# Kernel optimization log

Measured on AMD Instinct MI355X. Metric: run time of the kernel, lower is better.

The kernel has to match this reference:

```python
import jax, jax.numpy as jnp
import numpy as np

B, L, C, H = 32, 641, 768, 12
MEM = 128  # memory slots K; state token at index K; tokens are causal after that


def _block_mask(L, K):
    # rows i attend to cols j per FusedAttention:
    #  memory rows (i<K): attend to memory+state (j<=K)
    #  state row (i==K): attends to everything
    #  token rows (i>K): attend to memory+state (j<=K) and causally to tokens (K<j<=i)
    i = jnp.arange(L)[:, None]
    j = jnp.arange(L)[None, :]
    mem_rows = (i < K) & (j <= K)
    state_row = (i == K)
    tok_rows = (i > K) & ((j <= K) | ((j > K) & (j <= i)))
    return mem_rows | state_row | tok_rows  # (L, L) bool


def setup_inputs() -> dict:
    key = jax.random.key(0)
    k1, k2, k3 = jax.random.split(key, 3)
    x = jax.random.normal(k1, (B, L, C), dtype=jnp.float32)
    W_attn = jax.random.normal(k2, (C, 3 * C), dtype=jnp.float32) * 0.02
    W_proj = jax.random.normal(k3, (C, C), dtype=jnp.float32) * 0.02
    return {"x": x, "W_attn": W_attn, "W_proj": W_proj, "mem_size": MEM}


def reference(x, W_attn, W_proj, mem_size):
    Bb, Ll, Cc = x.shape
    hd = Cc // H
    qkv = x @ W_attn  # (B, L, 3C)
    q, k, v = jnp.split(qkv, 3, axis=-1)
    # (B, H, L, hd)
    q = q.reshape(Bb, Ll, H, hd).transpose(0, 2, 1, 3)
    k = k.reshape(Bb, Ll, H, hd).transpose(0, 2, 1, 3)
    v = v.reshape(Bb, Ll, H, hd).transpose(0, 2, 1, 3)
    mask = _block_mask(Ll, mem_size)  # (L, L)
    scale = 1.0 / jnp.sqrt(jnp.asarray(hd, dtype=x.dtype))
    att = jnp.einsum("bhqd,bhkd->bhqk", q, k) * scale
    att = jnp.where(mask[None, None, :, :], att, jnp.asarray(-jnp.inf, att.dtype))
    att = jax.nn.softmax(att, axis=-1)
    y = jnp.einsum("bhqk,bhkd->bhqd", att, v)
    y = y.transpose(0, 2, 1, 3).reshape(Bb, Ll, Cc)
    return y @ W_proj
```

## Files before the change

kernel.cpp:

```cpp
#include <hip/hip_runtime.h>
#include <stdint.h>

#define B_SZ 32
#define L_SZ 641
#define C_SZ 768
#define H_SZ 12
#define HD 64
#define MEMK 128
#define M_REAL (B_SZ * L_SZ)
#define M_PAD 20608
#define MT256 81
#define N_QKV (3 * C_SZ)
#define NQP 6
#define QK_STRIDE 1536
#define VT_STRIDE 648
#define SCL_LOG2E 0.18033688f
#define FIXED_MAX 8.0f

typedef __attribute__((ext_vector_type(8))) short short8;
typedef __attribute__((ext_vector_type(4))) float f32x4;
typedef __attribute__((ext_vector_type(4))) unsigned short ushort4v;

__device__ inline unsigned short f2bf(float x) {
  union { float f; uint32_t u; } v; v.f = x;
  uint32_t r = v.u + 0x7fffu + ((v.u >> 16) & 1u);
  return (unsigned short)(r >> 16);
}
__device__ inline float bf2f(short v) {
  union { float f; uint32_t u; } x; x.u = ((uint32_t)(unsigned short)v) << 16;
  return x.f;
}

__device__ inline void gload_lds16(const void* g, void* l) {
  __builtin_amdgcn_global_load_lds(
      (const __attribute__((address_space(1))) uint32_t*)g,
      (__attribute__((address_space(3))) uint32_t*)l, 16, 0, 0);
}

__global__ __launch_bounds__(256) void k_conv_x(const float* __restrict__ src,
                                                unsigned short* __restrict__ dst,
                                                int n4) {
  int i = blockIdx.x * 256 + threadIdx.x;
  if (i >= n4) return;
  float4 v = *(const float4*)(src + (size_t)i * 4);
  ushort4v o = { f2bf(v.x), f2bf(v.y), f2bf(v.z), f2bf(v.w) };
  int m = (unsigned)i / 192u;
  int k = (i - m * 192) * 4;
  int kk = k ^ ((m & 7) << 3);
  *(ushort4v*)(dst + (size_t)m * C_SZ + kk) = o;
}

__global__ __launch_bounds__(256) void k_transpose_bf16(const float* __restrict__ src,
                                                        unsigned short* __restrict__ dst,
                                                        int R, int Ccol,
                                                        float scale, int scale_cmax) {
  __shared__ float tile[32][33];
  int c0 = blockIdx.x * 32, r0 = blockIdx.y * 32;
  int tx = threadIdx.x & 31, ty = threadIdx.x >> 5;
  for (int i = ty; i < 32; i += 8)
    tile[i][tx] = src[(size_t)(r0 + i) * Ccol + c0 + tx];
  __syncthreads();
  float sc = (c0 < scale_cmax) ? scale : 1.0f;
  for (int i = ty; i < 32; i += 8) {
    int c = c0 + i;
    int r = (r0 + tx) ^ ((c & 7) << 3);
    dst[(size_t)c * R + r] = f2bf(tile[tx][i] * sc);
  }
}

template <int MODE>
__global__ __launch_bounds__(512, 2) void k_gemm(const short* __restrict__ A,
                                                 const short* __restrict__ Bt,
                                                 void* __restrict__ Cp,
                                                 short* __restrict__ vt,
                                                 int Mreal, int N, int K) {
  __shared__ short As[2][256 * 64];
  __shared__ short Bs[2][256 * 64];
  int nwg = gridDim.x;
  int qq = nwg >> 3, rr = nwg & 7;
  int x8 = blockIdx.x & 7, i8 = blockIdx.x >> 3;
  int wg = (x8 < rr ? x8 * (qq + 1) : rr * (qq + 1) + (x8 - rr) * qq) + i8;
  const int tiles_n = N >> 8;
  int tm = wg / tiles_n, tn = wg % tiles_n;
  int m0 = tm << 8, n0 = tn << 8;
  int tid = threadIdx.x;
  int lane = tid & 63, wave = tid >> 6;
  int wr = wave >> 2, wc = wave & 3;
  int l15 = lane & 15, g = lane >> 4;
  int gswz = (l15 & 7) << 4;

  f32x4 acc[8][4];
  f32x4 z = {0.f, 0.f, 0.f, 0.f};
#pragma unroll
  for (int i2 = 0; i2 < 8; ++i2)
#pragma unroll
    for (int j2 = 0; j2 < 4; ++j2) acc[i2][j2] = z;

  int srow = wave * 8 + (lane >> 3);
  int scol = (lane & 7) * 8;

#define STAGE(K0, BUF)                                                        \
  {                                                                           \
    _Pragma("unroll")                                                         \
    for (int s = 0; s < 4; ++s) {                                             \
      int ar = m0 + s * 64 + srow;                                            \
      if (ar >= M_PAD) ar = M_PAD - 1;      \
      gload_lds16(A + (size_t)ar * K + ((K0) + scol),                         \
                  (char*)As[BUF] + s * 8192 + wave * 1024);                   \
      gload_lds16(Bt + (size_t)(n0 + s * 64 + srow) * K + ((K0) + scol),      \
                  (char*)Bs[BUF] + s * 8192 + wave * 1024);                   \
    }                                                                         \
  }

  STAGE(0, 0);
  STAGE(64, 1);
  int nk = K >> 6;
  for (int t = 0; t < nk; ++t) {
    int buf = t & 1;
    if (t + 1 < nk) {
      asm volatile("s_waitcnt vmcnt(8)" ::: "memory");
    } else {
      asm volatile("s_waitcnt vmcnt(0)" ::: "memory");
    }
    __builtin_amdgcn_s_barrier();
#pragma unroll
    for (int ks = 0; ks < 2; ++ks) {
      short8 a[8], b[4];
      if (MODE == 3) {
#pragma unroll
        for (int j = 0; j < 8; ++j)
          a[j] = *(const short8*)((char*)Bs[buf] +
                      (wr * 128 + j * 16 + l15) * 128 + ((ks * 64 + g * 16) ^ gswz));
#pragma unroll
        for (int i = 0; i < 4; ++i)
          b[i] = *(const short8*)((char*)As[buf] +
                      (wc * 64 + i * 16 + l15) * 128 + ((ks * 64 + g * 16) ^ gswz));
      } else {
#pragma unroll
        for (int mf = 0; mf < 8; ++mf)
          a[mf] = *(const short8*)((char*)As[buf] +
                      (wr * 128 + mf * 16 + l15) * 128 + ((ks * 64 + g * 16) ^ gswz));
#pragma unroll
        for (int nf = 0; nf < 4; ++nf)
          b[nf] = *(const short8*)((char*)Bs[buf] +
                      (wc * 64 + nf * 16 + l15) * 128 + ((ks * 64 + g * 16) ^ gswz));
      }
#pragma unroll
      for (int i = 0; i < 8; ++i)
#pragma unroll
        for (int j = 0; j < 4; ++j)
          acc[i][j] = __builtin_amdgcn_mfma_f32_16x16x32_bf16(a[i], b[j], acc[i][j], 0, 0, 0);
    }
    __builtin_amdgcn_s_barrier();
    __builtin_amdgcn_sched_barrier(0);
    if (t + 2 < nk) STAGE((t + 2) << 6, buf);
  }
#undef STAGE

  if (MODE == 3) {
#pragma unroll
    for (int j = 0; j < 8; ++j) {
#pragma unroll
      for (int reg = 0; reg < 4; ++reg) {
        int n = n0 + wr * 128 + j * 16 + g * 4 + reg;
        int h = n >> 6, d = n & 63;
        int xr = (d & 7) << 3;
#pragma unroll
        for (int i = 0; i < 4; ++i) {
          int m = m0 + wc * 64 + i * 16 + l15;
          if (m >= Mreal) continue;
          int bb = (unsigned)m / 641u;
          int key = m - bb * 641;
          int k2 = (key >= 640) ? key : (key ^ xr);
          vt[((size_t)(bb * H_SZ + h) * HD + d) * VT_STRIDE + k2] = f2bf(acc[j][i][reg]);
        }
      }
    }
    return;
  }
#pragma unroll
  for (int mf = 0; mf < 8; ++mf) {
#pragma unroll
    for (int reg = 0; reg < 4; ++reg) {
      int m = m0 + wr * 128 + mf * 16 + g * 4 + reg;
      if (m >= Mreal) continue;
      int xr = 0;
      if (MODE == 2) {
        int bb = (unsigned)m / 641u;
        int key = m - bb * 641;
        xr = (key & 7) << 3;
      }
#pragma unroll
      for (int nf = 0; nf < 4; ++nf) {
        int n = n0 + wc * 64 + nf * 16 + l15;
        float v = acc[mf][nf][reg];
        if (MODE == 2) {
          int nn = (n >= C_SZ) ? (n ^ xr) : n;
          ((unsigned short*)Cp)[(size_t)m * QK_STRIDE + nn] = f2bf(v);
        } else
          ((float*)Cp)[(size_t)m * N + n] = v;
      }
    }
  }
}

__global__ __launch_bounds__(512) void k_attn(const short* __restrict__ qk,
                                              const short* __restrict__ vt,
                                              short* __restrict__ y) {
  __shared__ short Ks[2][64 * 64];
  __shared__ short Vt[2][64 * 64];
  __shared__ short Ps[8][16 * 64];

  int bid = blockIdx.x;
  int work = (bid & 7) * 288 + (bid >> 3);
  int qp = work % NQP;
  int rem = work / NQP;
  int h = rem % H_SZ;
  int b = rem / H_SZ;
  int q0 = qp * 128;
  int tid = threadIdx.x;
  int lane = tid & 63, w = tid >> 6;
  int wgp = w >> 2;
  int l15 = lane & 15, g = lane >> 4;
  int q0w = q0 + wgp * 64 + (w & 3) * 16;

  size_t qbase = (size_t)(b * L_SZ + q0w + l15) * QK_STRIDE + h * HD;
  short8 qa[2];
#pragma unroll
  for (int ks = 0; ks < 2; ++ks)
    qa[ks] = *(const short8*)&qk[qbase + ks * 32 + g * 8];

  f32x4 o[4];
  float l_run[4];
  f32x4 z = {0.f, 0.f, 0.f, 0.f};
  f32x4 m8 = {-FIXED_MAX, -FIXED_MAX, -FIXED_MAX, -FIXED_MAX};
#pragma unroll
  for (int df = 0; df < 4; ++df) o[df] = z;
#pragma unroll
  for (int r = 0; r < 4; ++r) l_run[r] = 0.f;

  int jmax[4];
#pragma unroll
  for (int reg = 0; reg < 4; ++reg) {
    int i = q0w + g * 4 + reg;
    jmax[reg] = (i == MEMK) ? (L_SZ - 1) : (i < MEMK ? MEMK : i);
  }
  int jm_min = (q0w <= MEMK) ? MEMK : q0w;

  int q1 = q0 + 127; if (q1 > L_SZ - 1) q1 = L_SZ - 1;
  int col_max = (q0 <= MEMK && MEMK <= q1) ? (L_SZ - 1) : (q1 < MEMK ? MEMK : q1);
  int qw1 = q0w + 15;
  bool dead = (q0w >= L_SZ);
  int wcol = (q0w <= MEMK && MEMK <= qw1) ? (L_SZ - 1) : (qw1 < MEMK ? MEMK : qw1);
  if (dead) wcol = -1;

  size_t kbase = (size_t)b * L_SZ * QK_STRIDE + C_SZ + h * HD;
  size_t vbase = (size_t)(b * H_SZ + h) * HD * VT_STRIDE;

  int i0 = tid >> 3, j0e = (tid & 7) * 8;
  int rswz = (l15 & 7) << 4;

#define STAGE_ATTN(C0, BUF)                                                   \
  {                                                                           \
    gload_lds16(qk + kbase + (size_t)((C0) + i0) * QK_STRIDE + j0e,           \
                (char*)Ks[BUF] + w * 1024);                                   \
    gload_lds16(vt + vbase + (size_t)i0 * VT_STRIDE + (C0) + j0e,             \
                (char*)Vt[BUF] + w * 1024);                                   \
  }

  STAGE_ATTN(0, 0);
  STAGE_ATTN(64, 1);

  int nt = col_max >> 6;
  for (int t = 0; t <= nt; ++t) {
    int c0 = t << 6;
    int buf = t & 1;
    if (t + 1 <= nt) {
      asm volatile("s_waitcnt vmcnt(2)" ::: "memory");
    } else {
      asm volatile("s_waitcnt vmcnt(0)" ::: "memory");
    }
    __builtin_amdgcn_s_barrier();

    if (c0 <= wcol) {
      int vswz = (c0 >= 640) ? 0 : rswz;

      f32x4 s[4];
      __builtin_amdgcn_s_setprio(1);
#pragma unroll
      for (int kf = 0; kf < 4; ++kf) {
        f32x4 sa = m8;
#pragma unroll
        for (int ks = 0; ks < 2; ++ks) {
          short8 kb = *(const short8*)((char*)Ks[buf] +
                          (kf * 16 + l15) * 128 + ((ks * 64 + g * 16) ^ rswz));
          sa = __builtin_amdgcn_mfma_f32_16x16x32_bf16(qa[ks], kb, sa, 0, 0, 0);
        }
        s[kf] = sa;
      }
      __builtin_amdgcn_s_setprio(0);

      if (c0 + 63 > jm_min) {
#pragma unroll
        for (int kf = 0; kf < 4; ++kf) {
          int j = c0 + kf * 16 + l15;
#pragma unroll
          for (int reg = 0; reg < 4; ++reg)
            s[kf][reg] = (j <= jmax[reg]) ? s[kf][reg] : -1e30f;
        }
      }

#pragma unroll
      for (int kf = 0; kf < 4; ++kf)
#pragma unroll
        for (int reg = 0; reg < 4; ++reg)
          s[kf][reg] = exp2f(s[kf][reg]);
#pragma unroll
      for (int reg = 0; reg < 4; ++reg)
        l_run[reg] += (s[0][reg] + s[1][reg]) + (s[2][reg] + s[3][reg]);

#pragma unroll
      for (int reg = 0; reg < 4; ++reg) {
        int q = g * 4 + reg;
        char* prow = (char*)Ps[w] + q * 128;
        int qswz = (q & 7) << 4;
#pragma unroll
        for (int kf = 0; kf < 4; kf += 2) {
          uint32_t r;
          asm("v_cvt_pk_bf16_f32 %0, %1, %2"
              : "=v"(r) : "v"(s[kf][reg]), "v"(s[kf + 1][reg]));
          *(short*)(prow + ((kf * 32 + l15 * 2) ^ qswz)) = (short)(r & 0xffff);
          *(short*)(prow + (((kf + 1) * 32 + l15 * 2) ^ qswz)) = (short)(r >> 16);
        }
      }

      short8 pa[2];
#pragma unroll
      for (int ks = 0; ks < 2; ++ks)
        pa[ks] = *(const short8*)((char*)Ps[w] + l15 * 128 + ((ks * 64 + g * 16) ^ rswz));
      __builtin_amdgcn_s_setprio(1);
#pragma unroll
      for (int df = 0; df < 4; ++df) {
#pragma unroll
        for (int ks = 0; ks < 2; ++ks) {
          short8 vb = *(const short8*)((char*)Vt[buf] +
                          (df * 16 + l15) * 128 + ((ks * 64 + g * 16) ^ vswz));
          o[df] = __builtin_amdgcn_mfma_f32_16x16x32_bf16(pa[ks], vb, o[df], 0, 0, 0);
        }
      }
      __builtin_amdgcn_s_setprio(0);
    }

    __builtin_amdgcn_s_barrier();
    __builtin_amdgcn_sched_barrier(0);
    if (t + 2 <= nt) STAGE_ATTN((t + 2) << 6, buf);
  }
#undef STAGE_ATTN

#pragma unroll
  for (int reg = 0; reg < 4; ++reg) {
    float ls = l_run[reg];
    ls += __shfl_xor(ls, 1);
    ls += __shfl_xor(ls, 2);
    ls += __shfl_xor(ls, 4);
    ls += __shfl_xor(ls, 8);
    int i = q0w + g * 4 + reg;
    if (i >= L_SZ) continue;
    float inv = 1.0f / ls;
    size_t m = (size_t)(b * L_SZ + i);
    int ixr = ((int)(m & 7)) << 3;
#pragma unroll
    for (int df = 0; df < 4; ++df) {
      int col = (df * 16 + l15) ^ ixr;
      y[m * C_SZ + h * HD + col] = (short)f2bf(o[df][reg] * inv);
    }
  }
}

extern "C" void kernel_launch(void* const* d_in, const int* in_sizes, int n_in,
                              void* d_out, int out_size, void* d_ws, size_t ws_size,
                              hipStream_t stream) {
  const float* x = (const float*)d_in[0];
  const float* Wa = (const float*)d_in[1];
  const float* Wp = (const float*)d_in[2];
  float* out = (float*)d_out;

  char* ws = (char*)d_ws;
  size_t off0 = 0;
  short* x_bf = (short*)(ws + off0);
  size_t off1 = off0 + (size_t)M_PAD * C_SZ * 2;
  short* Wa_t = (short*)(ws + off1);
  size_t off2 = off1 + (size_t)N_QKV * C_SZ * 2;
  short* Wp_t = (short*)(ws + off2);
  size_t off3 = off2 + (size_t)C_SZ * C_SZ * 2;
  short* qk = (short*)(ws + off3);
  size_t off4 = off3 + (size_t)M_REAL * QK_STRIDE * 2;
  short* vt = (short*)(ws + off4);
  size_t need = off4 + (size_t)B_SZ * H_SZ * HD * VT_STRIDE * 2 + 4096;
  if (ws_size < need) return;

  int n4 = M_REAL * C_SZ / 4;
  k_conv_x<<<(n4 + 255) / 256, 256, 0, stream>>>(x, (unsigned short*)x_bf, n4);
  k_transpose_bf16<<<dim3(N_QKV / 32, C_SZ / 32), 256, 0, stream>>>(
      Wa, (unsigned short*)Wa_t, C_SZ, N_QKV, SCL_LOG2E, C_SZ);
  k_transpose_bf16<<<dim3(C_SZ / 32, C_SZ / 32), 256, 0, stream>>>(
      Wp, (unsigned short*)Wp_t, C_SZ, C_SZ, 1.0f, 0);

  k_gemm<2><<<MT256 * (QK_STRIDE / 256), 512, 0, stream>>>(
      x_bf, Wa_t, (void*)qk, nullptr, M_REAL, QK_STRIDE, C_SZ);
  k_gemm<3><<<MT256 * (C_SZ / 256), 512, 0, stream>>>(
      x_bf, Wa_t + (size_t)QK_STRIDE * C_SZ, nullptr, vt, M_REAL, C_SZ, C_SZ);
  k_attn<<<B_SZ * H_SZ * NQP, 512, 0, stream>>>(qk, vt, x_bf );
  k_gemm<0><<<MT256 * (C_SZ / 256), 512, 0, stream>>>(
      x_bf, Wp_t, (void*)out, nullptr, M_REAL, C_SZ, C_SZ);
}
```

Before: 229.9 us.

## Balance attention work with load-balanced 16-row strips per wave across two blocks per head

Replaces the 6 query-tile blocks per (batch, head) with 2 blocks per head. Each wave processes up to three 16-row query strips chosen from a static table so that causal work is balanced across waves. K and V fragments are loaded from LDS once per 64-column tile and reused across a wave's strips, which removes load imbalance and redundant K/V staging. The cost is higher register pressure from three sets of accumulators, Q fragments and cached K/V, and fewer blocks (768), which may reduce occupancy and latency hiding.

```diff
diff --git a/kernel.cpp b/kernel.cpp
--- a/kernel.cpp
+++ b/kernel.cpp
@@ -11,7 +11,6 @@
 #define M_PAD 20608
 #define MT256 81
 #define N_QKV (3 * C_SZ)
-#define NQP 6
 #define QK_STRIDE 1536
 #define VT_STRIDE 648
 #define SCL_LOG2E 0.18033688f
@@ -36,6 +35,13 @@
       (const __attribute__((address_space(1))) uint32_t*)g,
       (__attribute__((address_space(3))) uint32_t*)l, 16, 0, 0);
 }
+
+static __device__ const int STRIPS[2][8][3] = {
+  { { 8, 12, 10}, {40, 14,  6}, {38, 16,  4}, {36, 18,  2},
+    {34, 20,  0}, {32, 22, -1}, {30, 24, -1}, {28, 26, -1} },
+  { {39,  9,  7}, {37, 11,  5}, {35, 13,  3}, {33, 15,  1},
+    {31, 17, -1}, {29, 19, -1}, {27, 21, -1}, {25, 23, -1} },
+};
 
 __global__ __launch_bounds__(256) void k_conv_x(const float* __restrict__ src,
                                                 unsigned short* __restrict__ dst,
@@ -212,47 +218,46 @@
   __shared__ short Ps[8][16 * 64];
 
   int bid = blockIdx.x;
-  int work = (bid & 7) * 288 + (bid >> 3);
-  int qp = work % NQP;
-  int rem = work / NQP;
-  int h = rem % H_SZ;
-  int b = rem / H_SZ;
-  int q0 = qp * 128;
+  int work = (bid & 7) * 96 + (bid >> 3);
+  int hb = work & 1;
+  int bh = work >> 1;
+  int h = bh % H_SZ;
+  int b = bh / H_SZ;
   int tid = threadIdx.x;
   int lane = tid & 63, w = tid >> 6;
-  int wgp = w >> 2;
   int l15 = lane & 15, g = lane >> 4;
-  int q0w = q0 + wgp * 64 + (w & 3) * 16;
-
-  size_t qbase = (size_t)(b * L_SZ + q0w + l15) * QK_STRIDE + h * HD;
-  short8 qa[2];
-#pragma unroll
-  for (int ks = 0; ks < 2; ++ks)
-    qa[ks] = *(const short8*)&qk[qbase + ks * 32 + g * 8];
-
-  f32x4 o[4];
-  float l_run[4];
+
+  int strip[3], wcol_s[3], jmin_s[3];
+  int jmax_s[3][4];
+  short8 qa_s[3][2];
+  f32x4 o_s[3][4];
+  float l_s[3][4];
   f32x4 z = {0.f, 0.f, 0.f, 0.f};
   f32x4 m8 = {-FIXED_MAX, -FIXED_MAX, -FIXED_MAX, -FIXED_MAX};
-#pragma unroll
-  for (int df = 0; df < 4; ++df) o[df] = z;
-#pragma unroll
-  for (int r = 0; r < 4; ++r) l_run[r] = 0.f;
-
-  int jmax[4];
-#pragma unroll
-  for (int reg = 0; reg < 4; ++reg) {
-    int i = q0w + g * 4 + reg;
-    jmax[reg] = (i == MEMK) ? (L_SZ - 1) : (i < MEMK ? MEMK : i);
-  }
-  int jm_min = (q0w <= MEMK) ? MEMK : q0w;
-
-  int q1 = q0 + 127; if (q1 > L_SZ - 1) q1 = L_SZ - 1;
-  int col_max = (q0 <= MEMK && MEMK <= q1) ? (L_SZ - 1) : (q1 < MEMK ? MEMK : q1);
-  int qw1 = q0w + 15;
-  bool dead = (q0w >= L_SZ);
-  int wcol = (q0w <= MEMK && MEMK <= qw1) ? (L_SZ - 1) : (qw1 < MEMK ? MEMK : qw1);
-  if (dead) wcol = -1;
+
+#pragma unroll
+  for (int k = 0; k < 3; ++k) {
+    int s = STRIPS[hb][w][k];
+    strip[k] = s;
+    int se = s < 0 ? 0 : s;
+    int r0 = se * 16;
+    size_t qb = (size_t)(b * L_SZ + r0 + l15) * QK_STRIDE + h * HD;
+#pragma unroll
+    for (int ks = 0; ks < 2; ++ks)
+      qa_s[k][ks] = *(const short8*)&qk[qb + ks * 32 + g * 8];
+#pragma unroll
+    for (int reg = 0; reg < 4; ++reg) {
+      int i = r0 + g * 4 + reg;
+      jmax_s[k][reg] = (i == MEMK) ? (L_SZ - 1) : (i < MEMK ? MEMK : i);
+      o_s[k][reg] = z;
+      l_s[k][reg] = 0.f;
+    }
+    jmin_s[k] = (r0 <= MEMK) ? MEMK : r0;
+    int qw1 = r0 + 15;
+    wcol_s[k] = (s < 0) ? -1
+                : ((r0 <= MEMK && MEMK <= qw1) ? (L_SZ - 1)
+                                               : (qw1 < MEMK ? MEMK : qw1));
+  }
 
   size_t kbase = (size_t)b * L_SZ * QK_STRIDE + C_SZ + h * HD;
   size_t vbase = (size_t)(b * H_SZ + h) * HD * VT_STRIDE;
@@ -271,6 +276,7 @@
   STAGE_ATTN(0, 0);
   STAGE_ATTN(64, 1);
 
+  int col_max = (L_SZ - 1) - hb;
   int nt = col_max >> 6;
   for (int t = 0; t <= nt; ++t) {
     int c0 = t << 6;
@@ -282,73 +288,82 @@
     }
     __builtin_amdgcn_s_barrier();
 
-    if (c0 <= wcol) {
+    if (c0 <= wcol_s[0] || c0 <= wcol_s[1] || c0 <= wcol_s[2]) {
       int vswz = (c0 >= 640) ? 0 : rswz;
-
-      f32x4 s[4];
-      __builtin_amdgcn_s_setprio(1);
-#pragma unroll
-      for (int kf = 0; kf < 4; ++kf) {
-        f32x4 sa = m8;
+      short8 kb[4][2], vb[4][2];
+#pragma unroll
+      for (int kf = 0; kf < 4; ++kf)
 #pragma unroll
         for (int ks = 0; ks < 2; ++ks) {
-          short8 kb = *(const short8*)((char*)Ks[buf] +
-                          (kf * 16 + l15) * 128 + ((ks * 64 + g * 16) ^ rswz));
-          sa = __builtin_amdgcn_mfma_f32_16x16x32_bf16(qa[ks], kb, sa, 0, 0, 0);
+          kb[kf][ks] = *(const short8*)((char*)Ks[buf] +
+                           (kf * 16 + l15) * 128 + ((ks * 64 + g * 16) ^ rswz));
+          vb[kf][ks] = *(const short8*)((char*)Vt[buf] +
+                           (kf * 16 + l15) * 128 + ((ks * 64 + g * 16) ^ vswz));
         }
-        s[kf] = sa;
-      }
-      __builtin_amdgcn_s_setprio(0);
-
-      if (c0 + 63 > jm_min) {
-#pragma unroll
-        for (int kf = 0; kf < 4; ++kf) {
-          int j = c0 + kf * 16 + l15;
+
+#pragma unroll
+      for (int k = 0; k < 3; ++k) {
+        if (c0 <= wcol_s[k]) {
+          f32x4 s[4];
+          __builtin_amdgcn_s_setprio(1);
+#pragma unroll
+          for (int kf = 0; kf < 4; ++kf) {
+            f32x4 sa = m8;
+#pragma unroll
+            for (int ks = 0; ks < 2; ++ks)
+              sa = __builtin_amdgcn_mfma_f32_16x16x32_bf16(qa_s[k][ks], kb[kf][ks], sa, 0, 0, 0);
+            s[kf] = sa;
+          }
+          __builtin_amdgcn_s_setprio(0);
+
+          if (c0 + 63 > jmin_s[k]) {
+#pragma unroll
+            for (int kf = 0; kf < 4; ++kf) {
+              int j = c0 + kf * 16 + l15;
+#pragma unroll
+              for (int reg = 0; reg < 4; ++reg)
+                s[kf][reg] = (j <= jmax_s[k][reg]) ? s[kf][reg] : -1e30f;
+            }
+          }
+
+#pragma unroll
+          for (int kf = 0; kf < 4; ++kf)
+#pragma unroll
+            for (int reg = 0; reg < 4; ++reg)
+              s[kf][reg] = exp2f(s[kf][reg]);
 #pragma unroll
           for (int reg = 0; reg < 4; ++reg)
-            s[kf][reg] = (j <= jmax[reg]) ? s[kf][reg] : -1e30f;
+            l_s[k][reg] += (s[0][reg] + s[1][reg]) + (s[2][reg] + s[3][reg]);
+
+#pragma unroll
+          for (int reg = 0; reg < 4; ++reg) {
+            int q = g * 4 + reg;
+            char* prow = (char*)Ps[w] + q * 128;
+            int qswz = (q & 7) << 4;
+#pragma unroll
+            for (int kf = 0; kf < 4; kf += 2) {
+              uint32_t r;
+              asm("v_cvt_pk_bf16_f32 %0, %1, %2"
+                  : "=v"(r) : "v"(s[kf][reg]), "v"(s[kf + 1][reg]));
+              *(short*)(prow + ((kf * 32 + l15 * 2) ^ qswz)) = (short)(r & 0xffff);
+              *(short*)(prow + (((kf + 1) * 32 + l15 * 2) ^ qswz)) = (short)(r >> 16);
+            }
+          }
+
+          short8 pa[2];
+#pragma unroll
+          for (int ks = 0; ks < 2; ++ks)
+            pa[ks] = *(const short8*)((char*)Ps[w] + l15 * 128 + ((ks * 64 + g * 16) ^ rswz));
+          __builtin_amdgcn_s_setprio(1);
+#pragma unroll
+          for (int df = 0; df < 4; ++df) {
+#pragma unroll
+            for (int ks = 0; ks < 2; ++ks)
+              o_s[k][df] = __builtin_amdgcn_mfma_f32_16x16x32_bf16(pa[ks], vb[df][ks], o_s[k][df], 0, 0, 0);
+          }
+          __builtin_amdgcn_s_setprio(0);
         }
       }
-
-#pragma unroll
-      for (int kf = 0; kf < 4; ++kf)
-#pragma unroll
-        for (int reg = 0; reg < 4; ++reg)
-          s[kf][reg] = exp2f(s[kf][reg]);
-#pragma unroll
-      for (int reg = 0; reg < 4; ++reg)
-        l_run[reg] += (s[0][reg] + s[1][reg]) + (s[2][reg] + s[3][reg]);
-
-#pragma unroll
-      for (int reg = 0; reg < 4; ++reg) {
-        int q = g * 4 + reg;
-        char* prow = (char*)Ps[w] + q * 128;
-        int qswz = (q & 7) << 4;
-#pragma unroll
-        for (int kf = 0; kf < 4; kf += 2) {
-          uint32_t r;
-          asm("v_cvt_pk_bf16_f32 %0, %1, %2"
-              : "=v"(r) : "v"(s[kf][reg]), "v"(s[kf + 1][reg]));
-          *(short*)(prow + ((kf * 32 + l15 * 2) ^ qswz)) = (short)(r & 0xffff);
-          *(short*)(prow + (((kf + 1) * 32 + l15 * 2) ^ qswz)) = (short)(r >> 16);
-        }
-      }
-
-      short8 pa[2];
-#pragma unroll
-      for (int ks = 0; ks < 2; ++ks)
-        pa[ks] = *(const short8*)((char*)Ps[w] + l15 * 128 + ((ks * 64 + g * 16) ^ rswz));
-      __builtin_amdgcn_s_setprio(1);
-#pragma unroll
-      for (int df = 0; df < 4; ++df) {
-#pragma unroll
-        for (int ks = 0; ks < 2; ++ks) {
-          short8 vb = *(const short8*)((char*)Vt[buf] +
-                          (df * 16 + l15) * 128 + ((ks * 64 + g * 16) ^ vswz));
-          o[df] = __builtin_amdgcn_mfma_f32_16x16x32_bf16(pa[ks], vb, o[df], 0, 0, 0);
-        }
-      }
-      __builtin_amdgcn_s_setprio(0);
     }
 
     __builtin_amdgcn_s_barrier();
@@ -358,21 +373,26 @@
 #undef STAGE_ATTN
 
 #pragma unroll
-  for (int reg = 0; reg < 4; ++reg) {
-    float ls = l_run[reg];
-    ls += __shfl_xor(ls, 1);
-    ls += __shfl_xor(ls, 2);
-    ls += __shfl_xor(ls, 4);
-    ls += __shfl_xor(ls, 8);
-    int i = q0w + g * 4 + reg;
-    if (i >= L_SZ) continue;
-    float inv = 1.0f / ls;
-    size_t m = (size_t)(b * L_SZ + i);
-    int ixr = ((int)(m & 7)) << 3;
-#pragma unroll
-    for (int df = 0; df < 4; ++df) {
-      int col = (df * 16 + l15) ^ ixr;
-      y[m * C_SZ + h * HD + col] = (short)f2bf(o[df][reg] * inv);
+  for (int k = 0; k < 3; ++k) {
+    if (strip[k] < 0) continue;
+    int r0 = strip[k] * 16;
+#pragma unroll
+    for (int reg = 0; reg < 4; ++reg) {
+      float ls = l_s[k][reg];
+      ls += __shfl_xor(ls, 1);
+      ls += __shfl_xor(ls, 2);
+      ls += __shfl_xor(ls, 4);
+      ls += __shfl_xor(ls, 8);
+      int i = r0 + g * 4 + reg;
+      if (i >= L_SZ) continue;
+      float inv = 1.0f / ls;
+      size_t m = (size_t)(b * L_SZ + i);
+      int ixr = ((int)(m & 7)) << 3;
+#pragma unroll
+      for (int df = 0; df < 4; ++df) {
+        int col = (df * 16 + l15) ^ ixr;
+        y[m * C_SZ + h * HD + col] = (short)f2bf(o_s[k][df][reg] * inv);
+      }
     }
   }
 }
@@ -410,7 +430,7 @@
       x_bf, Wa_t, (void*)qk, nullptr, M_REAL, QK_STRIDE, C_SZ);
   k_gemm<3><<<MT256 * (C_SZ / 256), 512, 0, stream>>>(
       x_bf, Wa_t + (size_t)QK_STRIDE * C_SZ, nullptr, vt, M_REAL, C_SZ, C_SZ);
-  k_attn<<<B_SZ * H_SZ * NQP, 512, 0, stream>>>(qk, vt, x_bf );
+  k_attn<<<B_SZ * H_SZ * 2, 512, 0, stream>>>(qk, vt, x_bf );
   k_gemm<0><<<MT256 * (C_SZ / 256), 512, 0, stream>>>(
       x_bf, Wp_t, (void*)out, nullptr, M_REAL, C_SZ, C_SZ);
 }
```

Result: slower. 236.7 us (+3.0%).

## Keep attention probabilities in registers by transposing the QK^T MFMA operands

Applied to the files above, without the earlier changes.

The QK^T MFMA now takes K as the A operand and Q as the B operand, so each lane holds scores for a single query row. The probabilities can then be packed straight into the PV MFMA operand in registers instead of going through a per-wave LDS buffer. V fragments are read as two 8-byte halves to match the new key ordering, and the masking and row-sum logic move to per-lane form. The output is transposed through reused K shared memory before the global store, which adds an extra LDS round trip in the epilogue.

```diff
diff --git a/kernel.cpp b/kernel.cpp
--- a/kernel.cpp
+++ b/kernel.cpp
@@ -18,6 +18,7 @@
 #define FIXED_MAX 8.0f
 
 typedef __attribute__((ext_vector_type(8))) short short8;
+typedef __attribute__((ext_vector_type(4))) short short4v;
 typedef __attribute__((ext_vector_type(4))) float f32x4;
 typedef __attribute__((ext_vector_type(4))) unsigned short ushort4v;
 
@@ -209,7 +210,6 @@
                                               short* __restrict__ y) {
   __shared__ short Ks[2][64 * 64];
   __shared__ short Vt[2][64 * 64];
-  __shared__ short Ps[8][16 * 64];
 
   int bid = blockIdx.x;
   int work = (bid & 7) * 288 + (bid >> 3);
@@ -231,20 +231,14 @@
     qa[ks] = *(const short8*)&qk[qbase + ks * 32 + g * 8];
 
   f32x4 o[4];
-  float l_run[4];
+  float l_run = 0.f;
   f32x4 z = {0.f, 0.f, 0.f, 0.f};
   f32x4 m8 = {-FIXED_MAX, -FIXED_MAX, -FIXED_MAX, -FIXED_MAX};
 #pragma unroll
   for (int df = 0; df < 4; ++df) o[df] = z;
-#pragma unroll
-  for (int r = 0; r < 4; ++r) l_run[r] = 0.f;
-
-  int jmax[4];
-#pragma unroll
-  for (int reg = 0; reg < 4; ++reg) {
-    int i = q0w + g * 4 + reg;
-    jmax[reg] = (i == MEMK) ? (L_SZ - 1) : (i < MEMK ? MEMK : i);
-  }
+
+  int i_lane = q0w + l15;
+  int jmax_lane = (i_lane == MEMK) ? (L_SZ - 1) : (i_lane < MEMK ? MEMK : i_lane);
   int jm_min = (q0w <= MEMK) ? MEMK : q0w;
 
   int q1 = q0 + 127; if (q1 > L_SZ - 1) q1 = L_SZ - 1;
@@ -294,7 +288,7 @@
         for (int ks = 0; ks < 2; ++ks) {
           short8 kb = *(const short8*)((char*)Ks[buf] +
                           (kf * 16 + l15) * 128 + ((ks * 64 + g * 16) ^ rswz));
-          sa = __builtin_amdgcn_mfma_f32_16x16x32_bf16(qa[ks], kb, sa, 0, 0, 0);
+          sa = __builtin_amdgcn_mfma_f32_16x16x32_bf16(kb, qa[ks], sa, 0, 0, 0);
         }
         s[kf] = sa;
       }
@@ -303,49 +297,42 @@
       if (c0 + 63 > jm_min) {
 #pragma unroll
         for (int kf = 0; kf < 4; ++kf) {
-          int j = c0 + kf * 16 + l15;
+          int jb = c0 + kf * 16 + g * 4;
 #pragma unroll
           for (int reg = 0; reg < 4; ++reg)
-            s[kf][reg] = (j <= jmax[reg]) ? s[kf][reg] : -1e30f;
+            s[kf][reg] = (jb + reg <= jmax_lane) ? s[kf][reg] : -1e30f;
         }
       }
 
 #pragma unroll
-      for (int kf = 0; kf < 4; ++kf)
+      for (int kf = 0; kf < 4; ++kf) {
 #pragma unroll
         for (int reg = 0; reg < 4; ++reg)
           s[kf][reg] = exp2f(s[kf][reg]);
-#pragma unroll
-      for (int reg = 0; reg < 4; ++reg)
-        l_run[reg] += (s[0][reg] + s[1][reg]) + (s[2][reg] + s[3][reg]);
-
-#pragma unroll
-      for (int reg = 0; reg < 4; ++reg) {
-        int q = g * 4 + reg;
-        char* prow = (char*)Ps[w] + q * 128;
-        int qswz = (q & 7) << 4;
-#pragma unroll
-        for (int kf = 0; kf < 4; kf += 2) {
-          uint32_t r;
-          asm("v_cvt_pk_bf16_f32 %0, %1, %2"
-              : "=v"(r) : "v"(s[kf][reg]), "v"(s[kf + 1][reg]));
-          *(short*)(prow + ((kf * 32 + l15 * 2) ^ qswz)) = (short)(r & 0xffff);
-          *(short*)(prow + (((kf + 1) * 32 + l15 * 2) ^ qswz)) = (short)(r >> 16);
-        }
+        l_run += (s[kf][0] + s[kf][1]) + (s[kf][2] + s[kf][3]);
       }
 
       short8 pa[2];
 #pragma unroll
-      for (int ks = 0; ks < 2; ++ks)
-        pa[ks] = *(const short8*)((char*)Ps[w] + l15 * 128 + ((ks * 64 + g * 16) ^ rswz));
+      for (int ks = 0; ks < 2; ++ks) {
+        union { uint32_t d[4]; short8 v; } u;
+        asm("v_cvt_pk_bf16_f32 %0, %1, %2" : "=v"(u.d[0]) : "v"(s[2 * ks][0]), "v"(s[2 * ks][1]));
+        asm("v_cvt_pk_bf16_f32 %0, %1, %2" : "=v"(u.d[1]) : "v"(s[2 * ks][2]), "v"(s[2 * ks][3]));
+        asm("v_cvt_pk_bf16_f32 %0, %1, %2" : "=v"(u.d[2]) : "v"(s[2 * ks + 1][0]), "v"(s[2 * ks + 1][1]));
+        asm("v_cvt_pk_bf16_f32 %0, %1, %2" : "=v"(u.d[3]) : "v"(s[2 * ks + 1][2]), "v"(s[2 * ks + 1][3]));
+        pa[ks] = u.v;
+      }
+
       __builtin_amdgcn_s_setprio(1);
 #pragma unroll
       for (int df = 0; df < 4; ++df) {
+        const char* vrow = (const char*)Vt[buf] + (df * 16 + l15) * 128;
 #pragma unroll
         for (int ks = 0; ks < 2; ++ks) {
-          short8 vb = *(const short8*)((char*)Vt[buf] +
-                          (df * 16 + l15) * 128 + ((ks * 64 + g * 16) ^ vswz));
-          o[df] = __builtin_amdgcn_mfma_f32_16x16x32_bf16(pa[ks], vb, o[df], 0, 0, 0);
+          union { short4v h[2]; short8 v; } vb;
+          vb.h[0] = *(const short4v*)(vrow + ((ks * 64 + g * 8) ^ vswz));
+          vb.h[1] = *(const short4v*)(vrow + ((ks * 64 + 32 + g * 8) ^ vswz));
+          o[df] = __builtin_amdgcn_mfma_f32_16x16x32_bf16(vb.v, pa[ks], o[df], 0, 0, 0);
         }
       }
       __builtin_amdgcn_s_setprio(0);
@@ -357,22 +344,33 @@
   }
 #undef STAGE_ATTN
 
-#pragma unroll
-  for (int reg = 0; reg < 4; ++reg) {
-    float ls = l_run[reg];
-    ls += __shfl_xor(ls, 1);
-    ls += __shfl_xor(ls, 2);
-    ls += __shfl_xor(ls, 4);
-    ls += __shfl_xor(ls, 8);
-    int i = q0w + g * 4 + reg;
+  float ls = l_run;
+  ls += __shfl_xor(ls, 16);
+  ls += __shfl_xor(ls, 32);
+  float inv = 1.0f / ls;
+
+  char* oreg = (char*)Ks[0] + w * 2048;
+  int wswz = (l15 & 7) << 4;
+#pragma unroll
+  for (int df = 0; df < 4; ++df)
+#pragma unroll
+    for (int reg = 0; reg < 4; ++reg)
+      *(short*)(oreg + l15 * 128 + (((df * 16 + g * 4 + reg) * 2) ^ wswz)) =
+          (short)f2bf(o[df][reg] * inv);
+  asm volatile("s_waitcnt lgkmcnt(0)" ::: "memory");
+
+#pragma unroll
+  for (int rr = 0; rr < 4; ++rr) {
+    int i = q0w + g * 4 + rr;
     if (i >= L_SZ) continue;
-    float inv = 1.0f / ls;
     size_t m = (size_t)(b * L_SZ + i);
     int ixr = ((int)(m & 7)) << 3;
+    int rsw2 = ((g * 4 + rr) & 7) << 4;
 #pragma unroll
     for (int df = 0; df < 4; ++df) {
+      short val = *(short*)(oreg + (g * 4 + rr) * 128 + (((df * 16 + l15) * 2) ^ rsw2));
       int col = (df * 16 + l15) ^ ixr;
-      y[m * C_SZ + h * HD + col] = (short)f2bf(o[df][reg] * inv);
+      y[m * C_SZ + h * HD + col] = val;
     }
   }
 }
```

After: 235.1 us (median of 2 runs). 1.02x slower.
